# Optimization experiments

Measured on AMD Instinct MI355X. Metric: run time of the kernel, lower is better.

## Reference

```python
import jax, jax.numpy as jnp
import numpy as np

NUM_HEADS = 16

def setup_inputs() -> dict:
    key = jax.random.key(0)
    k1, k2, k3 = jax.random.split(key, 3)
    B, N, D = 4, 2048, 1024
    init_attn_std = D ** (-0.5)
    x = jax.random.normal(k1, (B, N, D), dtype=jnp.float32)
    qkv_w = jax.random.normal(k2, (D, 3 * D), dtype=jnp.float32) * init_attn_std
    proj_w = jax.random.normal(k3, (D, D), dtype=jnp.float32) * init_attn_std
    proj_b = jnp.zeros((D,), dtype=jnp.float32)
    return {"x": x, "qkv_w": qkv_w, "proj_w": proj_w, "proj_b": proj_b}

def reference(x, qkv_w, proj_w, proj_b):
    B, N, D = x.shape
    H = NUM_HEADS
    hd = D // H
    scale = hd ** (-0.5)
    # QKV projection (no bias, qkv_bias=False)
    qkv = (x @ qkv_w).reshape(B, N, 3, H, hd)
    q, k, v = jnp.moveaxis(qkv, 2, 0)  # each [B, N, H, hd]
    # scaled dot-product attention with causal mask (matches flax nn.dot_product_attention)
    scores = jnp.einsum('bqhd,bkhd->bhqk', q * scale, k)  # [B, H, N, N]
    causal = jnp.tril(jnp.ones((N, N), dtype=bool))
    big_neg = jnp.finfo(scores.dtype).min
    scores = jnp.where(causal, scores, big_neg)
    attn = jax.nn.softmax(scores, axis=-1)
    out = jnp.einsum('bhqk,bkhd->bqhd', attn, v).reshape(B, N, D)
    # output projection (proj_bias=True)
    return out @ proj_w + proj_b
```

## Files before the change

kernel.cpp:

```cpp
#include <hip/hip_runtime.h>

typedef __attribute__((ext_vector_type(8))) short sh8;
typedef __attribute__((ext_vector_type(8))) __bf16 bf8v;
typedef __attribute__((ext_vector_type(4))) float f4v;
typedef __attribute__((ext_vector_type(16))) float f16v;
typedef __attribute__((ext_vector_type(4))) unsigned u4v;

__device__ __forceinline__ float fast_exp2(float x) { return __builtin_amdgcn_exp2f(x); }

__device__ __forceinline__ unsigned short f2bf(float f) {
  unsigned u = __builtin_bit_cast(unsigned, f);
  u += 0x7fffu + ((u >> 16) & 1u);
  return (unsigned short)(u >> 16);
}
__device__ __forceinline__ float bf2f(unsigned short h) {
  unsigned u = ((unsigned)h) << 16;
  return __builtin_bit_cast(float, u);
}

__device__ __forceinline__ void glds16(const unsigned short* g, unsigned short* l) {
  __builtin_amdgcn_global_load_lds((const __attribute__((address_space(1))) void*)g,
                                   (__attribute__((address_space(3))) void*)l, 16, 0, 0);
}

__global__ __launch_bounds__(256) void cast_kernel(const float* __restrict__ in,
                                                   unsigned short* __restrict__ out) {
  const int idx = (blockIdx.x * 256 + threadIdx.x) * 4;
  const float4 v = *(const float4*)(in + idx);
  ushort4 o;
  o.x = f2bf(v.x); o.y = f2bf(v.y); o.z = f2bf(v.z); o.w = f2bf(v.w);
  *(ushort4*)(out + idx) = o;
}

__global__ __launch_bounds__(256) void transpose_cast_kernel(const float* __restrict__ in,
                                                             unsigned short* __restrict__ out,
                                                             int R, int C) {
  __shared__ float tile[32][33];
  const int c0 = blockIdx.x * 32, r0 = blockIdx.y * 32;
  const int tx = threadIdx.x, ty = threadIdx.y;
#pragma unroll
  for (int i = 0; i < 4; ++i)
    tile[ty + 8 * i][tx] = in[(size_t)(r0 + ty + 8 * i) * C + c0 + tx];
  __syncthreads();
#pragma unroll
  for (int i = 0; i < 4; ++i)
    out[(size_t)(c0 + ty + 8 * i) * R + r0 + tx] = f2bf(tile[tx][ty + 8 * i]);
}

template <int MODE>
__global__ __launch_bounds__(256, 3) void gemm_bf16_kernel(
    const unsigned short* __restrict__ A,
    const unsigned short* __restrict__ Bt,
    int M, int N, int K,
    unsigned short* __restrict__ q_out, unsigned short* __restrict__ k_out,
    unsigned short* __restrict__ v_out,
    const float* __restrict__ bias, float* __restrict__ c_out) {
  __shared__ alignas(16) unsigned short As[3][128 * 32];
  __shared__ alignas(16) unsigned short Bs[3][128 * 32];
  const int tid = threadIdx.x;
  const int lane = tid & 63;
  const int wave = tid >> 6;
  const int wr = (wave >> 1) * 64;
  const int wc = (wave & 1) * 64;
  const int bm = blockIdx.x * 128;
  const int bn = blockIdx.y * 128;
  const int fr = lane & 15;
  const int kq = lane >> 4;

  f4v acc[4][4] = {};

  const int r16 = lane >> 2;
  const int srcsl = (lane & 3) ^ ((r16 >> 1) & 3);
  const int rb0 = wave * 32, rb1 = wave * 32 + 16;

#define GSTAGE(g, b)                                                                         \
  {                                                                                          \
    const int _k0 = (g) * 32;                                                                \
    glds16(&A[(size_t)(bm + rb0 + r16) * K + _k0 + srcsl * 8], &As[b][rb0 * 32]);            \
    glds16(&A[(size_t)(bm + rb1 + r16) * K + _k0 + srcsl * 8], &As[b][rb1 * 32]);            \
    glds16(&Bt[(size_t)(bn + rb0 + r16) * K + _k0 + srcsl * 8], &Bs[b][rb0 * 32]);           \
    glds16(&Bt[(size_t)(bn + rb1 + r16) * K + _k0 + srcsl * 8], &Bs[b][rb1 * 32]);           \
  }

  const int nT = K >> 5;
  GSTAGE(0, 0);
  GSTAGE(1, 1);

  const int rsl = (kq ^ ((fr >> 1) & 3)) * 8;

  int buf = 0;
  int bst = 2;
  for (int j = 0; j < nT; ++j) {
    if (j + 1 < nT) {
      asm volatile("s_waitcnt vmcnt(4)" ::: "memory");
    } else {
      asm volatile("s_waitcnt vmcnt(0)" ::: "memory");
    }
    __builtin_amdgcn_s_barrier();
    if (j + 2 < nT) GSTAGE(j + 2, bst);

    bf8v af[4], bfv[4];
#pragma unroll
    for (int m = 0; m < 4; ++m)
      af[m] = __builtin_bit_cast(bf8v, *(const sh8*)&As[buf][(wr + m * 16 + fr) * 32 + rsl]);
#pragma unroll
    for (int n = 0; n < 4; ++n)
      bfv[n] = __builtin_bit_cast(bf8v, *(const sh8*)&Bs[buf][(wc + n * 16 + fr) * 32 + rsl]);
    __builtin_amdgcn_s_setprio(1);
#pragma unroll
    for (int m = 0; m < 4; ++m)
#pragma unroll
      for (int n = 0; n < 4; ++n)
        acc[m][n] = __builtin_amdgcn_mfma_f32_16x16x32_bf16(af[m], bfv[n], acc[m][n], 0, 0, 0);
    __builtin_amdgcn_s_setprio(0);

    buf = (buf == 2) ? 0 : buf + 1;
    bst = (bst == 2) ? 0 : bst + 1;
  }
#undef GSTAGE

#pragma unroll
  for (int m = 0; m < 4; ++m) {
#pragma unroll
    for (int n = 0; n < 4; ++n) {
#pragma unroll
      for (int i = 0; i < 4; ++i) {
        const int r = bm + wr + m * 16 + kq * 4 + i;
        const int c = bn + wc + n * 16 + fr;
        const float val = acc[m][n][i];
        if (MODE == 0) {
          const int b = r >> 11, nidx = r & 2047;
          const int which = c >> 10, rem = c & 1023;
          const int h = rem >> 6, d = rem & 63;
          if (which == 0) {
            q_out[((size_t)((b * 16 + h) * 2048 + nidx)) * 64 + d] = f2bf(val * 0.18033688f);
          } else if (which == 1) {
            k_out[((size_t)((b * 16 + h) * 2048 + nidx)) * 64 + d] = f2bf(val);
          } else {
            v_out[((size_t)((b * 16 + h) * 64 + d)) * 2048 + nidx] = f2bf(val);
          }
        } else {
          c_out[(size_t)r * N + c] = val + bias[c];
        }
      }
    }
  }
}

__global__ __launch_bounds__(256, 2) void attn_kernel(
    const unsigned short* __restrict__ Q, const unsigned short* __restrict__ Kg,
    const unsigned short* __restrict__ Vtg, unsigned short* __restrict__ O) {
  __shared__ alignas(16) unsigned short Ks[4][64 * 64];
  __shared__ alignas(16) unsigned short Vts[4][64 * 64];
  const int tid = threadIdx.x;
  const int lane = tid & 63;
  const int w = tid >> 6;
  const int q31 = lane & 31, hi = lane >> 5;
  const int sw = (lane & 7) << 3;
  const int wg = (blockIdx.x & 7) * 64 + (blockIdx.x >> 3);
  const int bh = wg >> 3;
  const int pair = wg & 7;
  const int qtA = pair, qtB = 15 - pair;
  const unsigned short* Qb = Q + (size_t)bh * (2048 * 64);
  const unsigned short* Kb = Kg + (size_t)bh * (2048 * 64);
  const unsigned short* Vtb = Vtg + (size_t)bh * (64 * 2048);
  const int q0wA = qtA * 128 + w * 32;
  const int q0wB = qtB * 128 + w * 32;

  bf8v qfA[4], qfB[4];
#pragma unroll
  for (int dk = 0; dk < 4; ++dk) {
    qfA[dk] = __builtin_bit_cast(bf8v, *(const sh8*)&Qb[(size_t)(q0wA + q31) * 64 + 8 * hi + 16 * dk]);
    qfB[dk] = __builtin_bit_cast(bf8v, *(const sh8*)&Qb[(size_t)(q0wB + q31) * 64 + 8 * hi + 16 * dk]);
  }

  f16v oA0 = {}, oA1 = {}, oB0 = {}, oB1 = {};
  float mA = -1e30f, lA = 0.f, mB = -1e30f, lB = 0.f;

  const int r8 = lane >> 3;
  const int gslot = (lane & 7) ^ r8;
  const int rb0 = w * 16, rb1 = w * 16 + 8;

#define STAGE(g)                                                                              \
  {                                                                                           \
    const int _b = (g) & 3;                                                                   \
    glds16(&Kb[(size_t)((g) * 64 + rb0 + r8) * 64 + gslot * 8], &Ks[_b][rb0 * 64]);           \
    glds16(&Kb[(size_t)((g) * 64 + rb1 + r8) * 64 + gslot * 8], &Ks[_b][rb1 * 64]);           \
    glds16(&Vtb[(size_t)(rb0 + r8) * 2048 + (g) * 64 + gslot * 8], &Vts[_b][rb0 * 64]);       \
    glds16(&Vtb[(size_t)(rb1 + r8) * 2048 + (g) * 64 + gslot * 8], &Vts[_b][rb1 * 64]);       \
  }

  auto body = [&](int j, int buf, int q0w, bf8v (&qf)[4], f16v& o0, f16v& o1,
                  float& m_i, float& l_i) {
    f16v s0 = {}, s1 = {};
    __builtin_amdgcn_s_setprio(1);
#pragma unroll
    for (int dk = 0; dk < 4; ++dk) {
      const int col = (8 * hi + 16 * dk) ^ sw;
      const bf8v k0 = __builtin_bit_cast(bf8v, *(const sh8*)&Ks[buf][q31 * 64 + col]);
      const bf8v k1 = __builtin_bit_cast(bf8v, *(const sh8*)&Ks[buf][(32 + q31) * 64 + col]);
      s0 = __builtin_amdgcn_mfma_f32_32x32x16_bf16(k0, qf[dk], s0, 0, 0, 0);
      s1 = __builtin_amdgcn_mfma_f32_32x32x16_bf16(k1, qf[dk], s1, 0, 0, 0);
    }
    __builtin_amdgcn_s_setprio(0);

    const int qg = q0w + q31;
    if (j * 64 + 63 > q0w) {
#pragma unroll
      for (int r = 0; r < 16; ++r) {
        const int kl = j * 64 + (r & 3) + 8 * (r >> 2) + 4 * hi;
        if (kl > qg) s0[r] = -1e30f;
        if (kl + 32 > qg) s1[r] = -1e30f;
      }
    }

    float mx = -1e30f;
#pragma unroll
    for (int r = 0; r < 16; ++r) mx = fmaxf(mx, fmaxf(s0[r], s1[r]));
    mx = fmaxf(mx, __shfl_xor(mx, 32));

    if (!__all(mx - m_i <= 8.f)) {
      const float mn = fmaxf(m_i, mx);
      const float alpha = fast_exp2(m_i - mn);
      m_i = mn;
      l_i *= alpha;
#pragma unroll
      for (int r = 0; r < 16; ++r) {
        const float ar = __shfl(alpha, (r & 3) + 8 * (r >> 2) + 4 * hi);
        o0[r] *= ar;
        o1[r] *= ar;
      }
    }

    float ps = 0.f;
#pragma unroll
    for (int r = 0; r < 16; ++r) {
      s0[r] = fast_exp2(s0[r] - m_i);
      s1[r] = fast_exp2(s1[r] - m_i);
      ps += s0[r] + s1[r];
    }
    ps += __shfl_xor(ps, 32);
    l_i += ps;

    unsigned w0[8], w1[8];
#pragma unroll
    for (int jj = 0; jj < 8; ++jj) {
      asm("v_cvt_pk_bf16_f32 %0, %1, %2" : "=v"(w0[jj]) : "v"(s0[2 * jj]), "v"(s0[2 * jj + 1]));
      asm("v_cvt_pk_bf16_f32 %0, %1, %2" : "=v"(w1[jj]) : "v"(s1[2 * jj]), "v"(s1[2 * jj + 1]));
    }

#pragma unroll
    for (int ks = 0; ks < 4; ++ks) {
      const int j0 = 4 * (ks & 1);
      unsigned x0 = (ks < 2 ? w0[j0 + 0] : w1[j0 + 0]);
      unsigned y0 = (ks < 2 ? w0[j0 + 2] : w1[j0 + 2]);
      unsigned x1 = (ks < 2 ? w0[j0 + 1] : w1[j0 + 1]);
      unsigned y1 = (ks < 2 ? w0[j0 + 3] : w1[j0 + 3]);
      asm("v_permlane32_swap_b32 %0, %1" : "+v"(x0), "+v"(y0));
      asm("v_permlane32_swap_b32 %0, %1" : "+v"(x1), "+v"(y1));
      u4v pw;
      pw[0] = x0; pw[1] = x1; pw[2] = y0; pw[3] = y1;
      const bf8v pa = __builtin_bit_cast(bf8v, pw);

      const int colv = (8 * hi + 16 * ks) ^ sw;
      const bf8v vf0 = __builtin_bit_cast(bf8v, *(const sh8*)&Vts[buf][q31 * 64 + colv]);
      const bf8v vf1 = __builtin_bit_cast(bf8v, *(const sh8*)&Vts[buf][(32 + q31) * 64 + colv]);
      __builtin_amdgcn_s_setprio(1);
      o0 = __builtin_amdgcn_mfma_f32_32x32x16_bf16(pa, vf0, o0, 0, 0, 0);
      o1 = __builtin_amdgcn_mfma_f32_32x32x16_bf16(pa, vf1, o1, 0, 0, 0);
      __builtin_amdgcn_s_setprio(0);
    }
  };

  const int b = bh >> 4, h = bh & 15;
  auto epi = [&](int q0w, f16v& o0, f16v& o1, float l_i) {
    const float rl = 1.f / l_i;
#pragma unroll
    for (int r = 0; r < 16; ++r) {
      const int cr = (r & 3) + 8 * (r >> 2) + 4 * hi;
      const float lr = __shfl(rl, cr);
      const size_t base = ((size_t)(b * 2048 + q0w + cr)) * 1024 + h * 64 + q31;
      O[base] = f2bf(o0[r] * lr);
      O[base + 32] = f2bf(o1[r] * lr);
    }
  };

  const int nA = 2 * qtA + 2;
  const int nT = 2 * qtB + 2;

  STAGE(0);
  STAGE(1);

  for (int j = 0; j < nT; ++j) {
    const int buf = j & 3;
    if (j + 2 < nT) {
      STAGE(j + 2);
      asm volatile("s_waitcnt vmcnt(8)" ::: "memory");
    } else if (j + 1 < nT) {
      asm volatile("s_waitcnt vmcnt(4)" ::: "memory");
    } else {
      asm volatile("s_waitcnt vmcnt(0)" ::: "memory");
    }
    __builtin_amdgcn_s_barrier();

    if (j < nA) body(j, buf, q0wA, qfA, oA0, oA1, mA, lA);
    body(j, buf, q0wB, qfB, oB0, oB1, mB, lB);

    if (j == nA - 1) epi(q0wA, oA0, oA1, lA);
  }
#undef STAGE

  epi(q0wB, oB0, oB1, lB);
}

extern "C" void kernel_launch(void* const* d_in, const int* in_sizes, int n_in,
                              void* d_out, int out_size, void* d_ws, size_t ws_size,
                              hipStream_t stream) {
  const float* x      = (const float*)d_in[0];
  const float* qkv_w  = (const float*)d_in[1];
  const float* proj_w = (const float*)d_in[2];
  const float* proj_b = (const float*)d_in[3];
  float* out = (float*)d_out;

  unsigned short* ws = (unsigned short*)d_ws;
  const size_t NE = (size_t)8192 * 1024;
  unsigned short* xb     = ws;
  unsigned short* wqkvT  = xb + NE;
  unsigned short* wprojT = wqkvT + (size_t)3072 * 1024;
  unsigned short* qb     = wprojT + (size_t)1024 * 1024;
  unsigned short* kb     = qb + NE;
  unsigned short* vt     = kb + NE;
  unsigned short* ab     = xb;

  cast_kernel<<<8192, 256, 0, stream>>>(x, xb);
  transpose_cast_kernel<<<dim3(96, 32), dim3(32, 8), 0, stream>>>(qkv_w, wqkvT, 1024, 3072);
  transpose_cast_kernel<<<dim3(32, 32), dim3(32, 8), 0, stream>>>(proj_w, wprojT, 1024, 1024);

  gemm_bf16_kernel<0><<<dim3(64, 24), 256, 0, stream>>>(
      xb, wqkvT, 8192, 3072, 1024, qb, kb, vt, nullptr, nullptr);

  attn_kernel<<<512, 256, 0, stream>>>(qb, kb, vt, ab);

  gemm_bf16_kernel<1><<<dim3(64, 8), 256, 0, stream>>>(
      ab, wprojT, 8192, 1024, 1024, nullptr, nullptr, nullptr, proj_b, out);
}
```

Baseline: 185.8 us.

## Switch GEMM to BK=64 double-buffered LDS pipeline with 8-slot XOR swizzle

The bf16 GEMM K-tile grows from 32 to 64, and the triple-buffered pipeline with a partial vmcnt wait becomes double buffering with a full vmcnt(0) wait each iteration. LDS rows are now 64 elements wide with a 3-bit XOR swizzle, and each K-tile is consumed in two 32-wide halves. The goal is fewer barriers and loop iterations per unit of K, with larger loads per stage. In exchange, launch bounds drop to 2 blocks per CU because LDS per block rises, and a full wait before each stage may expose more global-load latency.

```diff
diff --git a/kernel.cpp b/kernel.cpp
--- a/kernel.cpp
+++ b/kernel.cpp
@@ -48,15 +48,15 @@
 }
 
 template <int MODE>
-__global__ __launch_bounds__(256, 3) void gemm_bf16_kernel(
+__global__ __launch_bounds__(256, 2) void gemm_bf16_kernel(
     const unsigned short* __restrict__ A,
     const unsigned short* __restrict__ Bt,
     int M, int N, int K,
     unsigned short* __restrict__ q_out, unsigned short* __restrict__ k_out,
     unsigned short* __restrict__ v_out,
     const float* __restrict__ bias, float* __restrict__ c_out) {
-  __shared__ alignas(16) unsigned short As[3][128 * 32];
-  __shared__ alignas(16) unsigned short Bs[3][128 * 32];
+  __shared__ alignas(16) unsigned short As[2][128 * 64];
+  __shared__ alignas(16) unsigned short Bs[2][128 * 64];
   const int tid = threadIdx.x;
   const int lane = tid & 63;
   const int wave = tid >> 6;
@@ -69,53 +69,47 @@
 
   f4v acc[4][4] = {};
 
-  const int r16 = lane >> 2;
-  const int srcsl = (lane & 3) ^ ((r16 >> 1) & 3);
-  const int rb0 = wave * 32, rb1 = wave * 32 + 16;
+  const int srow = lane >> 3;
+  const int sslot = (lane & 7) ^ srow;
 
 #define GSTAGE(g, b)                                                                         \
   {                                                                                          \
-    const int _k0 = (g) * 32;                                                                \
-    glds16(&A[(size_t)(bm + rb0 + r16) * K + _k0 + srcsl * 8], &As[b][rb0 * 32]);            \
-    glds16(&A[(size_t)(bm + rb1 + r16) * K + _k0 + srcsl * 8], &As[b][rb1 * 32]);            \
-    glds16(&Bt[(size_t)(bn + rb0 + r16) * K + _k0 + srcsl * 8], &Bs[b][rb0 * 32]);           \
-    glds16(&Bt[(size_t)(bn + rb1 + r16) * K + _k0 + srcsl * 8], &Bs[b][rb1 * 32]);           \
-  }
-
-  const int nT = K >> 5;
+    const int _k0 = (g) * 64;                                                                \
+    _Pragma("unroll")                                                                        \
+    for (int c = 0; c < 4; ++c) {                                                            \
+      const int rowbase = wave * 32 + c * 8;                                                 \
+      glds16(&A[(size_t)(bm + rowbase + srow) * K + _k0 + sslot * 8], &As[b][rowbase * 64]); \
+      glds16(&Bt[(size_t)(bn + rowbase + srow) * K + _k0 + sslot * 8], &Bs[b][rowbase * 64]);\
+    }                                                                                        \
+  }
+
+  const int nT = K >> 6;
   GSTAGE(0, 0);
-  GSTAGE(1, 1);
-
-  const int rsl = (kq ^ ((fr >> 1) & 3)) * 8;
-
-  int buf = 0;
-  int bst = 2;
+
   for (int j = 0; j < nT; ++j) {
-    if (j + 1 < nT) {
-      asm volatile("s_waitcnt vmcnt(4)" ::: "memory");
-    } else {
-      asm volatile("s_waitcnt vmcnt(0)" ::: "memory");
-    }
+    asm volatile("s_waitcnt vmcnt(0)" ::: "memory");
     __builtin_amdgcn_s_barrier();
-    if (j + 2 < nT) GSTAGE(j + 2, bst);
-
-    bf8v af[4], bfv[4];
-#pragma unroll
-    for (int m = 0; m < 4; ++m)
-      af[m] = __builtin_bit_cast(bf8v, *(const sh8*)&As[buf][(wr + m * 16 + fr) * 32 + rsl]);
-#pragma unroll
-    for (int n = 0; n < 4; ++n)
-      bfv[n] = __builtin_bit_cast(bf8v, *(const sh8*)&Bs[buf][(wc + n * 16 + fr) * 32 + rsl]);
-    __builtin_amdgcn_s_setprio(1);
-#pragma unroll
-    for (int m = 0; m < 4; ++m)
+    if (j + 1 < nT) GSTAGE(j + 1, (j + 1) & 1);
+    const int buf = j & 1;
+
+#pragma unroll
+    for (int h = 0; h < 2; ++h) {
+      bf8v af[4], bfv[4];
+      const int rsl = (((h << 2) | kq) ^ (fr & 7)) * 8;
+#pragma unroll
+      for (int m = 0; m < 4; ++m)
+        af[m] = __builtin_bit_cast(bf8v, *(const sh8*)&As[buf][(wr + m * 16 + fr) * 64 + rsl]);
 #pragma unroll
       for (int n = 0; n < 4; ++n)
-        acc[m][n] = __builtin_amdgcn_mfma_f32_16x16x32_bf16(af[m], bfv[n], acc[m][n], 0, 0, 0);
-    __builtin_amdgcn_s_setprio(0);
-
-    buf = (buf == 2) ? 0 : buf + 1;
-    bst = (bst == 2) ? 0 : bst + 1;
+        bfv[n] = __builtin_bit_cast(bf8v, *(const sh8*)&Bs[buf][(wc + n * 16 + fr) * 64 + rsl]);
+      __builtin_amdgcn_s_setprio(1);
+#pragma unroll
+      for (int m = 0; m < 4; ++m)
+#pragma unroll
+        for (int n = 0; n < 4; ++n)
+          acc[m][n] = __builtin_amdgcn_mfma_f32_16x16x32_bf16(af[m], bfv[n], acc[m][n], 0, 0, 0);
+      __builtin_amdgcn_s_setprio(0);
+    }
   }
 #undef GSTAGE
 
```

New measurement: 179.1 us. 3.6% less time.
